# Kernel tuning notes

Hardware: AMD Instinct MI355X
Metric: run time of the kernel (lower is better)

The kernel has to match this reference:

```python
import jax, jax.numpy as jnp
import numpy as np

B, S, D_IN, D_QK, D_V = 4, 4096, 1024, 64, 64

def setup_inputs() -> dict:
    key = jax.random.key(0)
    ks = jax.random.split(key, 8)
    sd = 1.0 / np.sqrt(D_IN)
    return {
        "X": jax.random.normal(ks[0], (B, S, D_IN), dtype=jnp.float32),
        "mask": jnp.ones((B, S, 1), dtype=jnp.float32),
        "Wq": jax.random.uniform(ks[1], (D_IN, D_QK), jnp.float32, -sd, sd),
        "bq": jax.random.uniform(ks[2], (D_QK,), jnp.float32, -sd, sd),
        "Wk": jax.random.uniform(ks[3], (D_IN, D_QK), jnp.float32, -sd, sd),
        "bk": jax.random.uniform(ks[4], (D_QK,), jnp.float32, -sd, sd),
        "Wv": jax.random.uniform(ks[5], (D_IN, D_V), jnp.float32, -sd, sd),
        "bv": jax.random.uniform(ks[6], (D_V,), jnp.float32, -sd, sd),
    }

def reference(X, mask, Wq, bq, Wk, bk, Wv, bv):
    # ReLU-activated projections (no head split, no 1/sqrt(d) scaling)
    q = jax.nn.relu(jnp.einsum('bsd,df->bsf', X, Wq) + bq)   # [B,S,D_QK]
    k = jax.nn.relu(jnp.einsum('bsd,df->bsf', X, Wk) + bk)   # [B,S,D_QK]
    v = jax.nn.relu(jnp.einsum('bsd,df->bsf', X, Wv) + bv)   # [B,S,D_V]
    scores = jax.nn.softmax(jnp.einsum('bqf,bkf->bqk', q, k), axis=-1)  # [B,S,S]
    return jnp.einsum('bqk,bkf->bqf', scores, v) * mask       # mask applied AFTER AV
```

## Files before the change

### kernel.cpp

```cpp
#include <hip/hip_runtime.h>


typedef short s16x8 __attribute__((ext_vector_type(8)));
typedef float fx4   __attribute__((ext_vector_type(4)));
typedef unsigned short u16x4 __attribute__((ext_vector_type(4)));

#define LOG2E 1.4426950408889634f

__device__ __forceinline__ unsigned short f2bf(float x) {
    unsigned int u = __float_as_uint(x);
    u += 0x7FFFu + ((u >> 16) & 1u);
    return (unsigned short)(u >> 16);
}
__device__ __forceinline__ float bf2f(unsigned short b) {
    return __uint_as_float(((unsigned int)b) << 16);
}

__global__ __launch_bounds__(256) void prep_w_kernel(
    const float* __restrict__ Wq, const float* __restrict__ Wk, const float* __restrict__ Wv,
    unsigned short* __restrict__ wt_hi, unsigned short* __restrict__ wt_lo)
{
    __shared__ __align__(16) unsigned short sh[64][72];
    __shared__ __align__(16) unsigned short sl[64][72];

    const int y  = blockIdx.x;
    const int kt = blockIdx.y;
    const float* W = (y == 0) ? Wq : (y == 1) ? Wk : Wv;
    const int t  = threadIdx.x;

    const int kl = t >> 2;
    const int c0 = (t & 3) * 16;
    const float* src = W + (size_t)(kt * 64 + kl) * 64 + c0;
    #pragma unroll
    for (int j = 0; j < 4; j++) {
        fx4 v = *(const fx4*)(src + j * 4);
        #pragma unroll
        for (int i = 0; i < 4; i++) {
            float x = v[i];
            unsigned short h = f2bf(x);
            unsigned short l = f2bf(x - bf2f(h));
            sh[c0 + j * 4 + i][kl] = h;
            sl[c0 + j * 4 + i][kl] = l;
        }
    }
    __syncthreads();

    const int c  = t >> 2;
    const int k0 = (t & 3) * 16;
    size_t o = (size_t)(y * 64 + c) * 1024 + kt * 64 + k0;
    *(s16x8*)(wt_hi + o)     = *(const s16x8*)&sh[c][k0];
    *(s16x8*)(wt_hi + o + 8) = *(const s16x8*)&sh[c][k0 + 8];
    *(s16x8*)(wt_lo + o)     = *(const s16x8*)&sl[c][k0];
    *(s16x8*)(wt_lo + o + 8) = *(const s16x8*)&sl[c][k0 + 8];
}

__global__ __launch_bounds__(768, 3) void proj_kernel(
    const float* __restrict__ X,
    const unsigned short* __restrict__ wt_hi, const unsigned short* __restrict__ wt_lo,
    const float* __restrict__ bq, const float* __restrict__ bk, const float* __restrict__ bv,
    unsigned short* __restrict__ q_hi, unsigned short* __restrict__ q_lo,
    unsigned short* __restrict__ k_bf, unsigned short* __restrict__ vt_g)
{
    __shared__ __align__(16) unsigned short a_hi[64][72];
    __shared__ __align__(16) unsigned short a_lo[64][72];
    __shared__ __align__(16) unsigned short bsh[192][72];
    __shared__ __align__(16) unsigned short bsl[192][72];

    const int tid  = threadIdx.x;
    const int lane = tid & 63;
    const int w    = tid >> 6;
    const int quad = lane >> 4;
    const int l15  = lane & 15;
    const int rowg = w & 1;
    const int colg = w >> 1;
    const int y    = colg >> 1;
    const int ch   = colg & 1;

    const int m0 = blockIdx.x * 64;

    fx4 acc[2][2];
    #pragma unroll
    for (int i = 0; i < 2; i++)
        #pragma unroll
        for (int j = 0; j < 2; j++) acc[i][j] = (fx4){0.f, 0.f, 0.f, 0.f};

    const int xrow = tid >> 4;
    const int xoff = (tid & 15) * 4;
    const float* xb0 = X + (size_t)(m0 + xrow) * 1024 + xoff;
    const float* xb1 = X + (size_t)(m0 + xrow + 32) * 1024 + xoff;

    const int wrow = tid >> 2;
    const int wk   = (tid & 3) * 16;
    const size_t wb = (size_t)wrow * 1024 + wk;

    fx4   xr[4][2];
    s16x8 wrh[2][2], wrl[2][2];
    if (tid < 512) {
        #pragma unroll
        for (int d = 0; d < 4; d++) {
            xr[d][0] = *(const fx4*)(xb0 + d * 64);
            xr[d][1] = *(const fx4*)(xb1 + d * 64);
        }
    }
    #pragma unroll
    for (int d = 0; d < 2; d++) {
        wrh[d][0] = *(const s16x8*)(wt_hi + wb + d * 64);
        wrh[d][1] = *(const s16x8*)(wt_hi + wb + d * 64 + 8);
        wrl[d][0] = *(const s16x8*)(wt_lo + wb + d * 64);
        wrl[d][1] = *(const s16x8*)(wt_lo + wb + d * 64 + 8);
    }

    #pragma unroll 4
    for (int kc = 0; kc < 16; kc++) {
        if (kc) __syncthreads();
        if (tid < 512) {
            #pragma unroll
            for (int i = 0; i < 2; i++) {
                fx4 xv = xr[kc & 3][i];
                unsigned short h0 = f2bf(xv.x), h1 = f2bf(xv.y), h2 = f2bf(xv.z), h3 = f2bf(xv.w);
                unsigned short l0 = f2bf(xv.x - bf2f(h0)), l1 = f2bf(xv.y - bf2f(h1));
                unsigned short l2 = f2bf(xv.z - bf2f(h2)), l3 = f2bf(xv.w - bf2f(h3));
                *(u16x4*)&a_hi[xrow + i * 32][xoff] = (u16x4){h0, h1, h2, h3};
                *(u16x4*)&a_lo[xrow + i * 32][xoff] = (u16x4){l0, l1, l2, l3};
            }
        }
        *(s16x8*)&bsh[wrow][wk]     = wrh[kc & 1][0];
        *(s16x8*)&bsh[wrow][wk + 8] = wrh[kc & 1][1];
        *(s16x8*)&bsl[wrow][wk]     = wrl[kc & 1][0];
        *(s16x8*)&bsl[wrow][wk + 8] = wrl[kc & 1][1];
        __syncthreads();

        if (tid < 512 && kc < 12) {
            xr[kc & 3][0] = *(const fx4*)(xb0 + (kc + 4) * 64);
            xr[kc & 3][1] = *(const fx4*)(xb1 + (kc + 4) * 64);
        }
        if (kc < 14) {
            wrh[kc & 1][0] = *(const s16x8*)(wt_hi + wb + (kc + 2) * 64);
            wrh[kc & 1][1] = *(const s16x8*)(wt_hi + wb + (kc + 2) * 64 + 8);
            wrl[kc & 1][0] = *(const s16x8*)(wt_lo + wb + (kc + 2) * 64);
            wrl[kc & 1][1] = *(const s16x8*)(wt_lo + wb + (kc + 2) * 64 + 8);
        }

        s16x8 ah[2][2], al[2][2];
        #pragma unroll
        for (int sub = 0; sub < 2; sub++)
            #pragma unroll
            for (int ks = 0; ks < 2; ks++) {
                const int r = rowg * 32 + sub * 16 + l15;
                ah[sub][ks] = *(const s16x8*)&a_hi[r][ks * 32 + quad * 8];
                al[sub][ks] = *(const s16x8*)&a_lo[r][ks * 32 + quad * 8];
            }
        #pragma unroll
        for (int nt = 0; nt < 2; nt++) {
            const int br = colg * 32 + nt * 16 + l15;
            #pragma unroll
            for (int ks = 0; ks < 2; ks++) {
                s16x8 bh = *(const s16x8*)&bsh[br][ks * 32 + quad * 8];
                s16x8 bl = *(const s16x8*)&bsl[br][ks * 32 + quad * 8];
                #pragma unroll
                for (int sub = 0; sub < 2; sub++) {
                    acc[sub][nt] = __builtin_amdgcn_mfma_f32_16x16x32_bf16(ah[sub][ks], bh, acc[sub][nt], 0, 0, 0);
                    acc[sub][nt] = __builtin_amdgcn_mfma_f32_16x16x32_bf16(ah[sub][ks], bl, acc[sub][nt], 0, 0, 0);
                    acc[sub][nt] = __builtin_amdgcn_mfma_f32_16x16x32_bf16(al[sub][ks], bh, acc[sub][nt], 0, 0, 0);
                }
            }
        }
    }
    __syncthreads();

    const float* bias = (y == 0) ? bq : (y == 1) ? bk : bv;
    const int b   = m0 >> 12;
    const int s0b = m0 & 4095;
    unsigned short* vtr = &a_hi[0][0];

    #pragma unroll
    for (int sub = 0; sub < 2; sub++)
        #pragma unroll
        for (int nt = 0; nt < 2; nt++) {
            const int col = ch * 32 + nt * 16 + l15;
            const float bb = bias[col];
            const int rloc = rowg * 32 + sub * 16 + quad * 4;
            #pragma unroll
            for (int r = 0; r < 4; r++) {
                float v = fmaxf(acc[sub][nt][r] + bb, 0.f);
                size_t grow = (size_t)(m0 + rloc + r);
                if (y == 0) {
                    unsigned short h = f2bf(v);
                    unsigned short l = f2bf(v - bf2f(h));
                    q_hi[grow * 64 + col] = h;
                    q_lo[grow * 64 + col] = l;
                } else if (y == 1) {
                    k_bf[grow * 64 + col] = f2bf(v);
                } else {
                    vtr[col * 72 + rloc + r] = f2bf(v);
                }
            }
        }
    __syncthreads();
    if (tid < 512) {
        int row = tid >> 3;
        int off = (tid & 7) * 8;
        s16x8 vv = *(const s16x8*)&vtr[row * 72 + off];
        *(s16x8*)(vt_g + (size_t)(b * 64 + row) * 4096 + s0b + off) = vv;
    }
}

__global__ __launch_bounds__(512, 6) void attn_kernel(
    const unsigned short* __restrict__ q_hi, const unsigned short* __restrict__ q_lo,
    const unsigned short* __restrict__ k_bf, const unsigned short* __restrict__ vt_g,
    unsigned short* __restrict__ pOb, float* __restrict__ pL)
{
    __shared__ __align__(16) unsigned short kt[64][72];
    __shared__ __align__(16) unsigned short vt[64][72];
    __shared__ __align__(16) unsigned short pt[8][16][40];

    const int tid  = threadIdx.x;
    const int lane = tid & 63;
    const int w    = tid >> 6;
    const int quad = lane >> 4;
    const int l15  = lane & 15;
    const int ck   = blockIdx.y;
    const int b    = blockIdx.z;
    const int q0   = blockIdx.x * 128;

    const size_t qoff = ((size_t)b * 4096 + q0 + w * 16 + l15) * 64 + quad * 8;
    s16x8 qh0 = *(const s16x8*)(q_hi + qoff);
    s16x8 qh1 = *(const s16x8*)(q_hi + qoff + 32);
    s16x8 ql0 = *(const s16x8*)(q_lo + qoff);
    s16x8 ql1 = *(const s16x8*)(q_lo + qoff + 32);

    fx4 accO[4];
    #pragma unroll
    for (int nt = 0; nt < 4; nt++) accO[nt] = (fx4){0.f, 0.f, 0.f, 0.f};
    float lsum[4] = {0.f, 0.f, 0.f, 0.f};

    const unsigned short* kgb = k_bf + (size_t)b * 4096 * 64;
    const unsigned short* vgb = vt_g + (size_t)b * 64 * 4096;

    const int srow = tid >> 3;
    const int soff = (tid & 7) * 8;

    const int it0 = ck * 8;
    s16x8 nk = *(const s16x8*)(kgb + (size_t)it0 * 4096 + (size_t)srow * 64 + soff);
    s16x8 nv = *(const s16x8*)(vgb + (size_t)srow * 4096 + it0 * 64 + soff);

    for (int it = it0; it < it0 + 8; it++) {
        *(s16x8*)&kt[srow][soff] = nk;
        *(s16x8*)&vt[srow][soff] = nv;
        __syncthreads();
        if (it + 1 < it0 + 8) {
            nk = *(const s16x8*)(kgb + (size_t)(it + 1) * 4096 + (size_t)srow * 64 + soff);
            nv = *(const s16x8*)(vgb + (size_t)srow * 4096 + (it + 1) * 64 + soff);
        }

        #pragma unroll
        for (int kh = 0; kh < 2; kh++) {
            #pragma unroll
            for (int nt2 = 0; nt2 < 2; nt2++) {
                int key = kh * 32 + nt2 * 16 + l15;
                s16x8 k0 = *(const s16x8*)&kt[key][quad * 8];
                s16x8 k1 = *(const s16x8*)&kt[key][32 + quad * 8];
                fx4 sc = (fx4){0.f, 0.f, 0.f, 0.f};
                __builtin_amdgcn_s_setprio(1);
                sc = __builtin_amdgcn_mfma_f32_16x16x32_bf16(qh0, k0, sc, 0, 0, 0);
                sc = __builtin_amdgcn_mfma_f32_16x16x32_bf16(ql0, k0, sc, 0, 0, 0);
                sc = __builtin_amdgcn_mfma_f32_16x16x32_bf16(qh1, k1, sc, 0, 0, 0);
                sc = __builtin_amdgcn_mfma_f32_16x16x32_bf16(ql1, k1, sc, 0, 0, 0);
                __builtin_amdgcn_s_setprio(0);
                #pragma unroll
                for (int r = 0; r < 4; r++) {
                    float p = __builtin_amdgcn_exp2f(sc[r] * LOG2E);
                    unsigned short pb = f2bf(p);
                    lsum[r] += bf2f(pb);
                    pt[w][quad * 4 + r][nt2 * 16 + l15] = pb;
                }
            }
            s16x8 pa = *(const s16x8*)&pt[w][l15][quad * 8];
            __builtin_amdgcn_s_setprio(1);
            #pragma unroll
            for (int nt = 0; nt < 4; nt++) {
                s16x8 vf = *(const s16x8*)&vt[nt * 16 + l15][kh * 32 + quad * 8];
                accO[nt] = __builtin_amdgcn_mfma_f32_16x16x32_bf16(pa, vf, accO[nt], 0, 0, 0);
            }
            __builtin_amdgcn_s_setprio(0);
        }
        __syncthreads();
    }

    #pragma unroll
    for (int r = 0; r < 4; r++) {
        float v = lsum[r];
        #pragma unroll
        for (int o = 1; o < 16; o <<= 1) v += __shfl_xor(v, o);
        lsum[r] = v;
    }
    #pragma unroll
    for (int r = 0; r < 4; r++) {
        int qrow = q0 + w * 16 + quad * 4 + r;
        size_t grow = (size_t)b * 4096 + qrow;
        #pragma unroll
        for (int nt = 0; nt < 4; nt++)
            pOb[((size_t)ck * 16384 + grow) * 64 + nt * 16 + l15] = f2bf(accO[nt][r]);
        if (l15 == 0)
            pL[(size_t)ck * 16384 + grow] = lsum[r];
    }
}

__global__ __launch_bounds__(256) void combine_kernel(
    const unsigned short* __restrict__ pOb, const float* __restrict__ pL,
    const float* __restrict__ mask, float* __restrict__ out)
{
    int idx = blockIdx.x * 256 + threadIdx.x;
    int q  = idx >> 4;
    int dg = idx & 15;
    fx4 s = (fx4){0.f, 0.f, 0.f, 0.f};
    float l = 0.f;
    #pragma unroll
    for (int c = 0; c < 8; c++) {
        u16x4 h = *(const u16x4*)(pOb + ((size_t)c * 16384 + q) * 64 + dg * 4);
        s.x += bf2f(h.x);
        s.y += bf2f(h.y);
        s.z += bf2f(h.z);
        s.w += bf2f(h.w);
        l += pL[(size_t)c * 16384 + q];
    }
    float scale = mask[q] / l;
    *(fx4*)(out + (size_t)q * 64 + dg * 4) = s * scale;
}

extern "C" void kernel_launch(void* const* d_in, const int* in_sizes, int n_in,
                              void* d_out, int out_size, void* d_ws, size_t ws_size,
                              hipStream_t stream)
{
    const float* X    = (const float*)d_in[0];
    const float* mask = (const float*)d_in[1];
    const float* Wq   = (const float*)d_in[2];
    const float* bq   = (const float*)d_in[3];
    const float* Wk   = (const float*)d_in[4];
    const float* bk   = (const float*)d_in[5];
    const float* Wv   = (const float*)d_in[6];
    const float* bv   = (const float*)d_in[7];
    float* out = (float*)d_out;

    char* ws = (char*)d_ws;
    unsigned short* q_hi  = (unsigned short*)(ws);
    unsigned short* q_lo  = (unsigned short*)(ws + (size_t)(2u << 20));
    unsigned short* k_bf  = (unsigned short*)(ws + (size_t)(4u << 20));
    unsigned short* vt_g  = (unsigned short*)(ws + (size_t)(6u << 20));
    unsigned short* wt_hi = (unsigned short*)(ws + (size_t)(8u << 20));
    unsigned short* wt_lo = (unsigned short*)(ws + (size_t)(8u << 20) + 393216);
    unsigned short* pOb   = (unsigned short*)(ws + (size_t)(9u << 20));
    float*          pL    = (float*)(ws + (size_t)(25u << 20));

    hipLaunchKernelGGL(prep_w_kernel, dim3(3, 16), dim3(256), 0, stream,
                       Wq, Wk, Wv, wt_hi, wt_lo);
    hipLaunchKernelGGL(proj_kernel, dim3(256), dim3(768), 0, stream,
                       X, wt_hi, wt_lo, bq, bk, bv, q_hi, q_lo, k_bf, vt_g);
    hipLaunchKernelGGL(attn_kernel, dim3(32, 8, 4), dim3(512), 0, stream,
                       q_hi, q_lo, k_bf, vt_g, pOb, pL);
    hipLaunchKernelGGL(combine_kernel, dim3(1024), dim3(256), 0, stream,
                       pOb, pL, mask, out);
}
```

Measured before the change: 166.3 us.

## Give each attention wave two 16-row query tiles and halve block size

The attention kernel now runs 4 waves of 256 threads instead of 8, and each wave handles 32 query rows as two 16-row sub-tiles. Every K and V fragment read from LDS feeds two sets of MFMAs, so LDS read traffic per FLOP is halved. The cost is more registers per wave (doubled Q fragments and accumulators), with launch bounds lowered to match. Fewer waves per block also means less latency hiding per barrier.

```diff
diff --git a/kernel.cpp b/kernel.cpp
--- a/kernel.cpp
+++ b/kernel.cpp
@@ -205,14 +205,14 @@
     }
 }
 
-__global__ __launch_bounds__(512, 6) void attn_kernel(
+__global__ __launch_bounds__(256, 3) void attn_kernel(
     const unsigned short* __restrict__ q_hi, const unsigned short* __restrict__ q_lo,
     const unsigned short* __restrict__ k_bf, const unsigned short* __restrict__ vt_g,
     unsigned short* __restrict__ pOb, float* __restrict__ pL)
 {
     __shared__ __align__(16) unsigned short kt[64][72];
     __shared__ __align__(16) unsigned short vt[64][72];
-    __shared__ __align__(16) unsigned short pt[8][16][40];
+    __shared__ __align__(16) unsigned short pt[4][32][40];
 
     const int tid  = threadIdx.x;
     const int lane = tid & 63;
@@ -223,16 +223,22 @@
     const int b    = blockIdx.z;
     const int q0   = blockIdx.x * 128;
 
-    const size_t qoff = ((size_t)b * 4096 + q0 + w * 16 + l15) * 64 + quad * 8;
-    s16x8 qh0 = *(const s16x8*)(q_hi + qoff);
-    s16x8 qh1 = *(const s16x8*)(q_hi + qoff + 32);
-    s16x8 ql0 = *(const s16x8*)(q_lo + qoff);
-    s16x8 ql1 = *(const s16x8*)(q_lo + qoff + 32);
-
-    fx4 accO[4];
-    #pragma unroll
-    for (int nt = 0; nt < 4; nt++) accO[nt] = (fx4){0.f, 0.f, 0.f, 0.f};
-    float lsum[4] = {0.f, 0.f, 0.f, 0.f};
+    const size_t qbase = ((size_t)b * 4096 + q0 + w * 32 + l15) * 64 + quad * 8;
+    s16x8 qh[2][2], ql[2][2];
+    #pragma unroll
+    for (int sub = 0; sub < 2; sub++) {
+        qh[sub][0] = *(const s16x8*)(q_hi + qbase + sub * 1024);
+        qh[sub][1] = *(const s16x8*)(q_hi + qbase + sub * 1024 + 32);
+        ql[sub][0] = *(const s16x8*)(q_lo + qbase + sub * 1024);
+        ql[sub][1] = *(const s16x8*)(q_lo + qbase + sub * 1024 + 32);
+    }
+
+    fx4 accO[2][4];
+    #pragma unroll
+    for (int sub = 0; sub < 2; sub++)
+        #pragma unroll
+        for (int nt = 0; nt < 4; nt++) accO[sub][nt] = (fx4){0.f, 0.f, 0.f, 0.f};
+    float lsum[2][4] = {{0.f, 0.f, 0.f, 0.f}, {0.f, 0.f, 0.f, 0.f}};
 
     const unsigned short* kgb = k_bf + (size_t)b * 4096 * 64;
     const unsigned short* vgb = vt_g + (size_t)b * 64 * 4096;
@@ -241,16 +247,22 @@
     const int soff = (tid & 7) * 8;
 
     const int it0 = ck * 8;
-    s16x8 nk = *(const s16x8*)(kgb + (size_t)it0 * 4096 + (size_t)srow * 64 + soff);
-    s16x8 nv = *(const s16x8*)(vgb + (size_t)srow * 4096 + it0 * 64 + soff);
+    s16x8 nk0 = *(const s16x8*)(kgb + (size_t)it0 * 4096 + (size_t)srow * 64 + soff);
+    s16x8 nk1 = *(const s16x8*)(kgb + (size_t)it0 * 4096 + (size_t)(srow + 32) * 64 + soff);
+    s16x8 nv0 = *(const s16x8*)(vgb + (size_t)srow * 4096 + it0 * 64 + soff);
+    s16x8 nv1 = *(const s16x8*)(vgb + (size_t)(srow + 32) * 4096 + it0 * 64 + soff);
 
     for (int it = it0; it < it0 + 8; it++) {
-        *(s16x8*)&kt[srow][soff] = nk;
-        *(s16x8*)&vt[srow][soff] = nv;
+        *(s16x8*)&kt[srow][soff]      = nk0;
+        *(s16x8*)&kt[srow + 32][soff] = nk1;
+        *(s16x8*)&vt[srow][soff]      = nv0;
+        *(s16x8*)&vt[srow + 32][soff] = nv1;
         __syncthreads();
         if (it + 1 < it0 + 8) {
-            nk = *(const s16x8*)(kgb + (size_t)(it + 1) * 4096 + (size_t)srow * 64 + soff);
-            nv = *(const s16x8*)(vgb + (size_t)srow * 4096 + (it + 1) * 64 + soff);
+            nk0 = *(const s16x8*)(kgb + (size_t)(it + 1) * 4096 + (size_t)srow * 64 + soff);
+            nk1 = *(const s16x8*)(kgb + (size_t)(it + 1) * 4096 + (size_t)(srow + 32) * 64 + soff);
+            nv0 = *(const s16x8*)(vgb + (size_t)srow * 4096 + (it + 1) * 64 + soff);
+            nv1 = *(const s16x8*)(vgb + (size_t)(srow + 32) * 4096 + (it + 1) * 64 + soff);
         }
 
         #pragma unroll
@@ -260,27 +272,32 @@
                 int key = kh * 32 + nt2 * 16 + l15;
                 s16x8 k0 = *(const s16x8*)&kt[key][quad * 8];
                 s16x8 k1 = *(const s16x8*)&kt[key][32 + quad * 8];
-                fx4 sc = (fx4){0.f, 0.f, 0.f, 0.f};
-                __builtin_amdgcn_s_setprio(1);
-                sc = __builtin_amdgcn_mfma_f32_16x16x32_bf16(qh0, k0, sc, 0, 0, 0);
-                sc = __builtin_amdgcn_mfma_f32_16x16x32_bf16(ql0, k0, sc, 0, 0, 0);
-                sc = __builtin_amdgcn_mfma_f32_16x16x32_bf16(qh1, k1, sc, 0, 0, 0);
-                sc = __builtin_amdgcn_mfma_f32_16x16x32_bf16(ql1, k1, sc, 0, 0, 0);
-                __builtin_amdgcn_s_setprio(0);
                 #pragma unroll
-                for (int r = 0; r < 4; r++) {
-                    float p = __builtin_amdgcn_exp2f(sc[r] * LOG2E);
-                    unsigned short pb = f2bf(p);
-                    lsum[r] += bf2f(pb);
-                    pt[w][quad * 4 + r][nt2 * 16 + l15] = pb;
+                for (int sub = 0; sub < 2; sub++) {
+                    fx4 sc = (fx4){0.f, 0.f, 0.f, 0.f};
+                    __builtin_amdgcn_s_setprio(1);
+                    sc = __builtin_amdgcn_mfma_f32_16x16x32_bf16(qh[sub][0], k0, sc, 0, 0, 0);
+                    sc = __builtin_amdgcn_mfma_f32_16x16x32_bf16(ql[sub][0], k0, sc, 0, 0, 0);
+                    sc = __builtin_amdgcn_mfma_f32_16x16x32_bf16(qh[sub][1], k1, sc, 0, 0, 0);
+                    sc = __builtin_amdgcn_mfma_f32_16x16x32_bf16(ql[sub][1], k1, sc, 0, 0, 0);
+                    __builtin_amdgcn_s_setprio(0);
+                    #pragma unroll
+                    for (int r = 0; r < 4; r++) {
+                        float p = __builtin_amdgcn_exp2f(sc[r] * LOG2E);
+                        unsigned short pb = f2bf(p);
+                        lsum[sub][r] += bf2f(pb);
+                        pt[w][sub * 16 + quad * 4 + r][nt2 * 16 + l15] = pb;
+                    }
                 }
             }
-            s16x8 pa = *(const s16x8*)&pt[w][l15][quad * 8];
+            s16x8 pa0 = *(const s16x8*)&pt[w][l15][quad * 8];
+            s16x8 pa1 = *(const s16x8*)&pt[w][16 + l15][quad * 8];
             __builtin_amdgcn_s_setprio(1);
             #pragma unroll
             for (int nt = 0; nt < 4; nt++) {
                 s16x8 vf = *(const s16x8*)&vt[nt * 16 + l15][kh * 32 + quad * 8];
-                accO[nt] = __builtin_amdgcn_mfma_f32_16x16x32_bf16(pa, vf, accO[nt], 0, 0, 0);
+                accO[0][nt] = __builtin_amdgcn_mfma_f32_16x16x32_bf16(pa0, vf, accO[0][nt], 0, 0, 0);
+                accO[1][nt] = __builtin_amdgcn_mfma_f32_16x16x32_bf16(pa1, vf, accO[1][nt], 0, 0, 0);
             }
             __builtin_amdgcn_s_setprio(0);
         }
@@ -288,22 +305,26 @@
     }
 
     #pragma unroll
-    for (int r = 0; r < 4; r++) {
-        float v = lsum[r];
-        #pragma unroll
-        for (int o = 1; o < 16; o <<= 1) v += __shfl_xor(v, o);
-        lsum[r] = v;
-    }
-    #pragma unroll
-    for (int r = 0; r < 4; r++) {
-        int qrow = q0 + w * 16 + quad * 4 + r;
-        size_t grow = (size_t)b * 4096 + qrow;
-        #pragma unroll
-        for (int nt = 0; nt < 4; nt++)
-            pOb[((size_t)ck * 16384 + grow) * 64 + nt * 16 + l15] = f2bf(accO[nt][r]);
-        if (l15 == 0)
-            pL[(size_t)ck * 16384 + grow] = lsum[r];
-    }
+    for (int sub = 0; sub < 2; sub++)
+        #pragma unroll
+        for (int r = 0; r < 4; r++) {
+            float v = lsum[sub][r];
+            #pragma unroll
+            for (int o = 1; o < 16; o <<= 1) v += __shfl_xor(v, o);
+            lsum[sub][r] = v;
+        }
+    #pragma unroll
+    for (int sub = 0; sub < 2; sub++)
+        #pragma unroll
+        for (int r = 0; r < 4; r++) {
+            int qrow = q0 + w * 32 + sub * 16 + quad * 4 + r;
+            size_t grow = (size_t)b * 4096 + qrow;
+            #pragma unroll
+            for (int nt = 0; nt < 4; nt++)
+                pOb[((size_t)ck * 16384 + grow) * 64 + nt * 16 + l15] = f2bf(accO[sub][nt][r]);
+            if (l15 == 0)
+                pL[(size_t)ck * 16384 + grow] = lsum[sub][r];
+        }
 }
 
 __global__ __launch_bounds__(256) void combine_kernel(
@@ -356,7 +377,7 @@
                        Wq, Wk, Wv, wt_hi, wt_lo);
     hipLaunchKernelGGL(proj_kernel, dim3(256), dim3(768), 0, stream,
                        X, wt_hi, wt_lo, bq, bk, bv, q_hi, q_lo, k_bf, vt_g);
-    hipLaunchKernelGGL(attn_kernel, dim3(32, 8, 4), dim3(512), 0, stream,
+    hipLaunchKernelGGL(attn_kernel, dim3(32, 8, 4), dim3(256), 0, stream,
                        q_hi, q_lo, k_bf, vt_g, pOb, pL);
     hipLaunchKernelGGL(combine_kernel, dim3(1024), dim3(256), 0, stream,
                        pOb, pL, mask, out);
```

Result: no change. 167.1 us (+0.4%).
